# Optimization experiments

Measured on AMD Instinct MI355X. Metric: run time of the kernel, lower is better.

## Reference

```python
import jax, jax.numpy as jnp
import numpy as np

NUM_HEADS = 32
NUM_KV_HEADS = 8
HEAD_DIM = 128
SEQ = 2048
MAX_SLOTS = 4096
SCALE = float(1.0 / np.sqrt(HEAD_DIM))  # attn_scale
G = NUM_HEADS // NUM_KV_HEADS  # num_queries_per_kv


def setup_inputs() -> dict:
    key = jax.random.key(0)
    k1, k2, k3 = jax.random.split(key, 3)
    q = jax.random.normal(k1, (SEQ, NUM_HEADS, HEAD_DIM), dtype=jnp.float32)
    k = jax.random.normal(k2, (SEQ, NUM_KV_HEADS, HEAD_DIM), dtype=jnp.float32)
    v = jax.random.normal(k3, (SEQ, NUM_KV_HEADS, HEAD_DIM), dtype=jnp.float32)
    k_cache = jnp.zeros((MAX_SLOTS, NUM_KV_HEADS, HEAD_DIM), dtype=jnp.float32)
    v_cache = jnp.zeros((MAX_SLOTS, NUM_KV_HEADS, HEAD_DIM), dtype=jnp.float32)
    slot_mapping = jnp.arange(SEQ, dtype=jnp.int64)  # contiguous block_table slots
    return {"q": q, "k": k, "v": v, "k_cache": k_cache, "v_cache": v_cache,
            "slot_mapping": slot_mapping}


def reference(q, k, v, k_cache, v_cache, slot_mapping):
    # prefill: scatter-write new K/V into the paged cache (self.k_cache[slot_mapping] = k)
    kc = k_cache.at[slot_mapping].set(k)
    vc = v_cache.at[slot_mapping].set(v)
    # gather K/V back from the cache via slot mapping (paged gather pattern)
    k_attn = kc[slot_mapping]  # (S, Hkv, D) == k since slots are unique
    v_attn = vc[slot_mapping]
    # GQA: repeat_interleave kv heads to match query heads
    kr = jnp.repeat(k_attn, G, axis=1)  # (S, H, D)
    vr = jnp.repeat(v_attn, G, axis=1)
    # scores: (H, Sq, Sk), naive full materialization as in the original
    scores = jnp.einsum('qhd,khd->hqk', q, kr) * SCALE
    sq, sk = q.shape[0], k_attn.shape[0]
    mask = jnp.tril(jnp.ones((sq, sk), dtype=bool))  # causal (num_query_tokens > 1)
    scores = jnp.where(mask[None, :, :], scores, -jnp.inf)
    weights = jax.nn.softmax(scores, axis=-1)
    out = jnp.einsum('hqk,khd->qhd', weights, vr)  # (S, H, D)
    return out
```

## Files before the change

### kernel.cpp

```cpp
#include <hip/hip_runtime.h>
#include <hip/hip_bf16.h>

#define QSTRIDE 4096
#define KSTRIDE 1024
#define CSCALE 0.1275174364688796f

typedef __attribute__((ext_vector_type(8))) short short8;
typedef __attribute__((ext_vector_type(4))) float f32x4;

union S8U { short8 s; unsigned u[4]; };

__device__ __forceinline__ unsigned short f2bf(float f) {
    union { __hip_bfloat16 b; unsigned short u; } cv;
    cv.b = __float2bfloat16(f);
    return cv.u;
}

__launch_bounds__(256, 3)
__global__ void attn_fwd(const float* __restrict__ Qg,
                         const float* __restrict__ Kg,
                         const float* __restrict__ Vg,
                         float* __restrict__ Og) {
    const int bid = blockIdx.x;
    const int qb  = 31 - (bid >> 5);
    const int h   = bid & 31;
    const int hk  = h >> 2;
    const int tid  = threadIdx.x;
    const int w    = tid >> 6;
    const int lane = tid & 63;
    const int c16  = lane & 15;
    const int g    = lane >> 4;
    const int dg   = g * 8;

    __shared__ unsigned short Ks[64][136];
    __shared__ unsigned short Vt[128][72];

    const int q0w  = qb * 64 + w * 16;
    const int qrow = q0w + c16;

    short8 qf[4];
    {
        const float* qp = Qg + (size_t)qrow * QSTRIDE + h * 128 + dg;
        #pragma unroll
        for (int ks = 0; ks < 4; ++ks) {
            f32x4 a = *(const f32x4*)(qp + ks * 32);
            f32x4 b = *(const f32x4*)(qp + ks * 32 + 4);
            short8 f;
            f[0] = (short)f2bf(a[0] * CSCALE); f[1] = (short)f2bf(a[1] * CSCALE);
            f[2] = (short)f2bf(a[2] * CSCALE); f[3] = (short)f2bf(a[3] * CSCALE);
            f[4] = (short)f2bf(b[0] * CSCALE); f[5] = (short)f2bf(b[1] * CSCALE);
            f[6] = (short)f2bf(b[2] * CSCALE); f[7] = (short)f2bf(b[3] * CSCALE);
            qf[ks] = f;
        }
    }

    const int ka  = tid >> 5;
    const int kc  = (tid & 31) * 4;
    const int va  = tid & 15;
    const int vch = tid >> 4;

    f32x4 kreg[8], vreg[8];

    auto LOAD_T = [&](int t) {
        const float* kb = Kg + (size_t)(t * 64) * KSTRIDE + hk * 128;
        const float* vb = Vg + (size_t)(t * 64) * KSTRIDE + hk * 128;
        #pragma unroll
        for (int it = 0; it < 8; ++it)
            kreg[it] = *(const f32x4*)(kb + (ka + 8 * it) * KSTRIDE + kc);
        #pragma unroll
        for (int task = 0; task < 2; ++task) {
            #pragma unroll
            for (int j = 0; j < 4; ++j)
                vreg[task * 4 + j] =
                    *(const f32x4*)(vb + (4 * va + j) * KSTRIDE + (vch + 16 * task) * 4);
        }
    };

    auto WRITE_T = [&]() {
        #pragma unroll
        for (int it = 0; it < 8; ++it) {
            ushort4 u = make_ushort4(f2bf(kreg[it][0]), f2bf(kreg[it][1]),
                                     f2bf(kreg[it][2]), f2bf(kreg[it][3]));
            *(ushort4*)&Ks[ka + 8 * it][kc] = u;
        }
        #pragma unroll
        for (int task = 0; task < 2; ++task) {
            const int d0 = 4 * (vch + 16 * task);
            #pragma unroll
            for (int di = 0; di < 4; ++di) {
                ushort4 u = make_ushort4(f2bf(vreg[task * 4 + 0][di]),
                                         f2bf(vreg[task * 4 + 1][di]),
                                         f2bf(vreg[task * 4 + 2][di]),
                                         f2bf(vreg[task * 4 + 3][di]));
                *(ushort4*)&Vt[d0 + di][4 * va] = u;
            }
        }
    };

    f32x4 oacc[8];
    #pragma unroll
    for (int dt = 0; dt < 8; ++dt) oacc[dt] = (f32x4){0.f, 0.f, 0.f, 0.f};
    float m = -1e30f, l = 0.f;

    const int nt = qb + 1;
    LOAD_T(0);
    WRITE_T();
    if (nt > 1) LOAD_T(1);
    __syncthreads();

    for (int t = 0; t < nt; ++t) {
        const int kv0 = t * 64;

        f32x4 sacc[4];
        __builtin_amdgcn_s_setprio(1);
        #pragma unroll
        for (int ct = 0; ct < 4; ++ct) {
            f32x4 acc = (f32x4){0.f, 0.f, 0.f, 0.f};
            #pragma unroll
            for (int ks = 0; ks < 4; ++ks) {
                short8 kf = *(const short8*)&Ks[ct * 16 + c16][ks * 32 + dg];
                acc = __builtin_amdgcn_mfma_f32_16x16x32_bf16(kf, qf[ks], acc, 0, 0, 0);
            }
            sacc[ct] = acc;
        }
        __builtin_amdgcn_s_setprio(0);

        const bool needmask = (kv0 + 63) > q0w;
        float mx = -1e30f;
        #pragma unroll
        for (int ct = 0; ct < 4; ++ct) {
            #pragma unroll
            for (int r = 0; r < 4; ++r) {
                float s = sacc[ct][r];
                const int kv = kv0 + ct * 16 + 4 * g + r;
                if (needmask && kv > qrow) s = -1e30f;
                sacc[ct][r] = s;
                mx = fmaxf(mx, s);
            }
        }
        mx = fmaxf(mx, __shfl_xor(mx, 16));
        mx = fmaxf(mx, __shfl_xor(mx, 32));

        const float mn  = fmaxf(m, mx);
        const float fac = exp2f(m - mn);
        m = mn;

        float ps = 0.f;
        #pragma unroll
        for (int ct = 0; ct < 4; ++ct) {
            #pragma unroll
            for (int r = 0; r < 4; ++r) {
                float p = exp2f(sacc[ct][r] - m);
                sacc[ct][r] = p;
                ps += p;
            }
        }
        ps += __shfl_xor(ps, 16);
        ps += __shfl_xor(ps, 32);
        l = l * fac + ps;

        #pragma unroll
        for (int dt = 0; dt < 8; ++dt) {
            #pragma unroll
            for (int r = 0; r < 4; ++r) oacc[dt][r] *= fac;
        }

        unsigned pk[4][2];
        #pragma unroll
        for (int ct = 0; ct < 4; ++ct) {
            #pragma unroll
            for (int j = 0; j < 2; ++j)
                pk[ct][j] = (unsigned)f2bf(sacc[ct][2 * j]) |
                            ((unsigned)f2bf(sacc[ct][2 * j + 1]) << 16);
        }
        S8U pf0, pf1;
        {
            const int sb = ((g & 1) << 5) | c16;
            #pragma unroll
            for (int b = 0; b < 2; ++b) {
                const int src = sb + (b << 4);
                #pragma unroll
                for (int j = 0; j < 2; ++j) {
                    unsigned lo0 = (unsigned)__shfl((int)pk[0][j], src);
                    unsigned hi0 = (unsigned)__shfl((int)pk[1][j], src);
                    unsigned lo1 = (unsigned)__shfl((int)pk[2][j], src);
                    unsigned hi1 = (unsigned)__shfl((int)pk[3][j], src);
                    pf0.u[2 * b + j] = (g & 2) ? hi0 : lo0;
                    pf1.u[2 * b + j] = (g & 2) ? hi1 : lo1;
                }
            }
        }

        __builtin_amdgcn_s_setprio(1);
        #pragma unroll
        for (int dt = 0; dt < 8; ++dt) {
            short8 vfa = *(const short8*)&Vt[dt * 16 + c16][0 * 32 + dg];
            short8 vfb = *(const short8*)&Vt[dt * 16 + c16][1 * 32 + dg];
            oacc[dt] = __builtin_amdgcn_mfma_f32_16x16x32_bf16(vfa, pf0.s, oacc[dt], 0, 0, 0);
            oacc[dt] = __builtin_amdgcn_mfma_f32_16x16x32_bf16(vfb, pf1.s, oacc[dt], 0, 0, 0);
        }
        __builtin_amdgcn_s_setprio(0);

        if (t + 1 < nt) {
            __syncthreads();
            WRITE_T();
            if (t + 2 < nt) LOAD_T(t + 2);
            __syncthreads();
        }
    }

    const float rl = 1.0f / l;
    float* op = Og + (size_t)qrow * QSTRIDE + h * 128 + 4 * g;
    #pragma unroll
    for (int dt = 0; dt < 8; ++dt) {
        float4 o;
        o.x = oacc[dt][0] * rl; o.y = oacc[dt][1] * rl;
        o.z = oacc[dt][2] * rl; o.w = oacc[dt][3] * rl;
        *(float4*)(op + dt * 16) = o;
    }
}

extern "C" void kernel_launch(void* const* d_in, const int* in_sizes, int n_in,
                              void* d_out, int out_size, void* d_ws, size_t ws_size,
                              hipStream_t stream) {
    const float* q = (const float*)d_in[0];
    const float* k = (const float*)d_in[1];
    const float* v = (const float*)d_in[2];
    float* out = (float*)d_out;
    attn_fwd<<<dim3(1024), 256, 0, stream>>>(q, k, v, out);
}
```

Measured before the change: 104.1 us.

## Pre-convert K/V to bf16, use 32x32 MFMA with 128-row query tiles and async LDS loads

Two prep kernels convert K to bf16 in head-major layout and V to a transposed bf16 layout in the workspace. The attention kernel then uses 128-query blocks with 32x32x16 MFMAs and streams K/V tiles into swizzled double-buffered LDS via global_load_lds. It also adds a lazy rescale that skips the softmax correction when the running max barely changes, and an LDS-staged coalesced output store. The aim is to remove the repeated fp32 K/V loads and per-block conversion, and to raise MFMA efficiency. In exchange it adds two extra launches and workspace traffic, and occupancy drops to 2 blocks per CU.

```diff
diff --git a/kernel.cpp b/kernel.cpp
--- a/kernel.cpp
+++ b/kernel.cpp
@@ -1,14 +1,16 @@
 #include <hip/hip_runtime.h>
 #include <hip/hip_bf16.h>
 
-#define QSTRIDE 4096
-#define KSTRIDE 1024
+#define SEQ 2048
+#define QSTR 4096
+#define KSTR 1024
 #define CSCALE 0.1275174364688796f
 
-typedef __attribute__((ext_vector_type(8))) short short8;
-typedef __attribute__((ext_vector_type(4))) float f32x4;
-
-union S8U { short8 s; unsigned u[4]; };
+typedef __attribute__((ext_vector_type(8)))  short short8;
+typedef __attribute__((ext_vector_type(4)))  float f32x4;
+typedef __attribute__((ext_vector_type(16))) float f32x16;
+
+union PF8 { unsigned u[4]; short8 s; };
 
 __device__ __forceinline__ unsigned short f2bf(float f) {
     union { __hip_bfloat16 b; unsigned short u; } cv;
@@ -16,207 +18,267 @@
     return cv.u;
 }
 
-__launch_bounds__(256, 3)
+__device__ __forceinline__ void gload16(const unsigned short* g, unsigned short* l) {
+    __builtin_amdgcn_global_load_lds(
+        (const __attribute__((address_space(1))) void*)g,
+        (__attribute__((address_space(3))) void*)l, 16, 0, 0);
+}
+
+__global__ void prep_k(const float* __restrict__ Kg, unsigned short* __restrict__ Kb) {
+    int gi = blockIdx.x * 256 + threadIdx.x;
+    int kv = gi >> 8;
+    int rem = gi & 255;
+    int hk = rem >> 5;
+    int d4 = rem & 31;
+    f32x4 k4 = *(const f32x4*)(Kg + ((size_t)kv * 8 + hk) * 128 + 4 * d4);
+    ushort4 u = make_ushort4(f2bf(k4[0]), f2bf(k4[1]), f2bf(k4[2]), f2bf(k4[3]));
+    *(ushort4*)(Kb + ((size_t)hk * SEQ + kv) * 128 + 4 * d4) = u;
+}
+
+__global__ void prep_v(const float* __restrict__ Vg, unsigned short* __restrict__ Vtb) {
+    const int hk  = blockIdx.x >> 5;
+    const int kvb = blockIdx.x & 31;
+    __shared__ unsigned short T[128][72];
+    const int t = threadIdx.x;
+    #pragma unroll
+    for (int i = 0; i < 8; ++i) {
+        int idx = t + 256 * i;
+        int r = idx >> 5, d4 = idx & 31;
+        f32x4 v = *(const f32x4*)(Vg + ((size_t)(kvb * 64 + r) * 8 + hk) * 128 + 4 * d4);
+        T[4 * d4 + 0][r] = f2bf(v[0]);
+        T[4 * d4 + 1][r] = f2bf(v[1]);
+        T[4 * d4 + 2][r] = f2bf(v[2]);
+        T[4 * d4 + 3][r] = f2bf(v[3]);
+    }
+    __syncthreads();
+    #pragma unroll
+    for (int i = 0; i < 8; ++i) {
+        int idx = t + 256 * i;
+        int d = idx >> 4, c4 = idx & 15;
+        ushort4 u = *(ushort4*)&T[d][4 * c4];
+        *(ushort4*)(Vtb + ((size_t)hk * 128 + d) * SEQ + kvb * 64 + 4 * c4) = u;
+    }
+}
+
+__launch_bounds__(256, 2)
 __global__ void attn_fwd(const float* __restrict__ Qg,
-                         const float* __restrict__ Kg,
-                         const float* __restrict__ Vg,
+                         const unsigned short* __restrict__ Kb,
+                         const unsigned short* __restrict__ Vtb,
                          float* __restrict__ Og) {
-    const int bid = blockIdx.x;
-    const int qb  = 31 - (bid >> 5);
-    const int h   = bid & 31;
-    const int hk  = h >> 2;
+    const int bid  = blockIdx.x;
+    const int gidx = bid >> 5;
+    const int qb   = (gidx < 8) ? (15 - gidx) : (gidx - 8);
+    const int h    = bid & 31;
+    const int hk   = h >> 2;
     const int tid  = threadIdx.x;
     const int w    = tid >> 6;
     const int lane = tid & 63;
-    const int c16  = lane & 15;
-    const int g    = lane >> 4;
-    const int dg   = g * 8;
-
-    __shared__ unsigned short Ks[64][136];
-    __shared__ unsigned short Vt[128][72];
-
-    const int q0w  = qb * 64 + w * 16;
-    const int qrow = q0w + c16;
-
-    short8 qf[4];
+    const int q5   = lane & 31;
+    const int t5   = lane >> 5;
+    const int swz  = lane & 7;
+
+    __shared__ __align__(16) unsigned char smem[67584];
+    typedef unsigned short KsT[64][128];
+    typedef unsigned short VtT[128][64];
+    KsT* Ks = (KsT*)smem;
+    VtT* Vt = (VtT*)(smem + 32768);
+    float (*Ot)[132] = (float(*)[132])smem;
+
+    const int q0w = qb * 128 + 32 * w;
+    const int nt  = 2 * qb + 2;
+
+    short8 qf[8];
     {
-        const float* qp = Qg + (size_t)qrow * QSTRIDE + h * 128 + dg;
-        #pragma unroll
-        for (int ks = 0; ks < 4; ++ks) {
-            f32x4 a = *(const f32x4*)(qp + ks * 32);
-            f32x4 b = *(const f32x4*)(qp + ks * 32 + 4);
+        const float* qp = Qg + (size_t)(q0w + q5) * QSTR + h * 128 + 8 * t5;
+        #pragma unroll
+        for (int st = 0; st < 8; ++st) {
+            f32x4 a = *(const f32x4*)(qp + 16 * st);
+            f32x4 b = *(const f32x4*)(qp + 16 * st + 4);
             short8 f;
             f[0] = (short)f2bf(a[0] * CSCALE); f[1] = (short)f2bf(a[1] * CSCALE);
             f[2] = (short)f2bf(a[2] * CSCALE); f[3] = (short)f2bf(a[3] * CSCALE);
             f[4] = (short)f2bf(b[0] * CSCALE); f[5] = (short)f2bf(b[1] * CSCALE);
             f[6] = (short)f2bf(b[2] * CSCALE); f[7] = (short)f2bf(b[3] * CSCALE);
-            qf[ks] = f;
-        }
-    }
-
-    const int ka  = tid >> 5;
-    const int kc  = (tid & 31) * 4;
-    const int va  = tid & 15;
-    const int vch = tid >> 4;
-
-    f32x4 kreg[8], vreg[8];
-
-    auto LOAD_T = [&](int t) {
-        const float* kb = Kg + (size_t)(t * 64) * KSTRIDE + hk * 128;
-        const float* vb = Vg + (size_t)(t * 64) * KSTRIDE + hk * 128;
-        #pragma unroll
-        for (int it = 0; it < 8; ++it)
-            kreg[it] = *(const f32x4*)(kb + (ka + 8 * it) * KSTRIDE + kc);
-        #pragma unroll
-        for (int task = 0; task < 2; ++task) {
-            #pragma unroll
-            for (int j = 0; j < 4; ++j)
-                vreg[task * 4 + j] =
-                    *(const f32x4*)(vb + (4 * va + j) * KSTRIDE + (vch + 16 * task) * 4);
+            qf[st] = f;
+        }
+    }
+    #pragma unroll
+    for (int st = 0; st < 8; ++st) asm volatile("" :: "v"(qf[st]));
+    asm volatile("s_waitcnt vmcnt(0)" ::: "memory");
+
+    f32x16 oacc[4];
+    #pragma unroll
+    for (int dt = 0; dt < 4; ++dt)
+        #pragma unroll
+        for (int r = 0; r < 16; ++r) oacc[dt][r] = 0.f;
+    float m = -1e30f, l = 0.f;
+
+    auto ISSUE = [&](int t, int b) {
+        const int kv0 = t * 64;
+        #pragma unroll
+        for (int p = 0; p < 4; ++p) {
+            int row = 16 * w + 4 * p + (lane >> 4);
+            const unsigned short* g = Kb +
+                ((size_t)hk * SEQ + kv0 + row) * 128 + 8 * ((lane & 15) ^ (row & 7));
+            gload16(g, &Ks[b][16 * w + 4 * p][0]);
+        }
+        #pragma unroll
+        for (int p = 0; p < 4; ++p) {
+            int d = 32 * w + 8 * p + (lane >> 3);
+            const unsigned short* g = Vtb +
+                ((size_t)hk * 128 + d) * SEQ + kv0 + 8 * ((lane & 7) ^ (d & 7));
+            gload16(g, &Vt[b][32 * w + 8 * p][0]);
         }
     };
 
-    auto WRITE_T = [&]() {
-        #pragma unroll
-        for (int it = 0; it < 8; ++it) {
-            ushort4 u = make_ushort4(f2bf(kreg[it][0]), f2bf(kreg[it][1]),
-                                     f2bf(kreg[it][2]), f2bf(kreg[it][3]));
-            *(ushort4*)&Ks[ka + 8 * it][kc] = u;
-        }
-        #pragma unroll
-        for (int task = 0; task < 2; ++task) {
-            const int d0 = 4 * (vch + 16 * task);
-            #pragma unroll
-            for (int di = 0; di < 4; ++di) {
-                ushort4 u = make_ushort4(f2bf(vreg[task * 4 + 0][di]),
-                                         f2bf(vreg[task * 4 + 1][di]),
-                                         f2bf(vreg[task * 4 + 2][di]),
-                                         f2bf(vreg[task * 4 + 3][di]));
-                *(ushort4*)&Vt[d0 + di][4 * va] = u;
-            }
-        }
-    };
-
-    f32x4 oacc[8];
-    #pragma unroll
-    for (int dt = 0; dt < 8; ++dt) oacc[dt] = (f32x4){0.f, 0.f, 0.f, 0.f};
-    float m = -1e30f, l = 0.f;
-
-    const int nt = qb + 1;
-    LOAD_T(0);
-    WRITE_T();
-    if (nt > 1) LOAD_T(1);
-    __syncthreads();
+    ISSUE(0, 0);
+    if (nt > 1) ISSUE(1, 1);
 
     for (int t = 0; t < nt; ++t) {
         const int kv0 = t * 64;
-
-        f32x4 sacc[4];
-        __builtin_amdgcn_s_setprio(1);
-        #pragma unroll
-        for (int ct = 0; ct < 4; ++ct) {
-            f32x4 acc = (f32x4){0.f, 0.f, 0.f, 0.f};
+        const int buf = t & 1;
+        if (t + 1 < nt) asm volatile("s_waitcnt vmcnt(8)" ::: "memory");
+        else            asm volatile("s_waitcnt vmcnt(0)" ::: "memory");
+        __builtin_amdgcn_s_barrier();
+
+        const bool active = (kv0 <= q0w + 31);
+        if (active) {
+            f32x16 sac[2];
+            __builtin_amdgcn_s_setprio(1);
+            #pragma unroll
+            for (int kvs = 0; kvs < 2; ++kvs) {
+                f32x16 acc;
+                #pragma unroll
+                for (int r = 0; r < 16; ++r) acc[r] = 0.f;
+                #pragma unroll
+                for (int st = 0; st < 8; ++st) {
+                    short8 kf = *(const short8*)
+                        &Ks[buf][32 * kvs + q5][8 * ((2 * st + t5) ^ swz)];
+                    acc = __builtin_amdgcn_mfma_f32_32x32x16_bf16(kf, qf[st], acc, 0, 0, 0);
+                }
+                sac[kvs] = acc;
+            }
+            __builtin_amdgcn_s_setprio(0);
+
+            if (kv0 + 63 > q0w) {
+                const int qrow = q0w + q5;
+                #pragma unroll
+                for (int kvs = 0; kvs < 2; ++kvs)
+                    #pragma unroll
+                    for (int r = 0; r < 16; ++r) {
+                        int kv = kv0 + 32 * kvs + (r & 3) + 8 * (r >> 2) + 4 * t5;
+                        if (kv > qrow) sac[kvs][r] = -1e30f;
+                    }
+            }
+
+            float mx = sac[0][0];
+            #pragma unroll
+            for (int kvs = 0; kvs < 2; ++kvs)
+                #pragma unroll
+                for (int r = 0; r < 16; ++r) mx = fmaxf(mx, sac[kvs][r]);
+            mx = fmaxf(mx, __shfl_xor(mx, 32));
+
+            const bool skip = __all(mx <= m + 11.0f);
+            float fac = 1.0f;
+            if (!skip) {
+                float mn = fmaxf(m, mx);
+                fac = exp2f(m - mn);
+                m = mn;
+            }
+
+            float ps = 0.f;
+            #pragma unroll
+            for (int kvs = 0; kvs < 2; ++kvs)
+                #pragma unroll
+                for (int r = 0; r < 16; ++r) {
+                    float p = exp2f(sac[kvs][r] - m);
+                    sac[kvs][r] = p;
+                    ps += p;
+                }
+            ps += __shfl_xor(ps, 32);
+            if (!skip) {
+                l = l * fac + ps;
+                #pragma unroll
+                for (int dt = 0; dt < 4; ++dt)
+                    #pragma unroll
+                    for (int r = 0; r < 16; ++r) oacc[dt][r] *= fac;
+            } else {
+                l += ps;
+            }
+
+            unsigned pkw[2][8];
+            #pragma unroll
+            for (int a = 0; a < 2; ++a)
+                #pragma unroll
+                for (int rp = 0; rp < 8; ++rp)
+                    pkw[a][rp] = (unsigned)f2bf(sac[a][2 * rp]) |
+                                 ((unsigned)f2bf(sac[a][2 * rp + 1]) << 16);
+
+            unsigned xp[2][8];
+            #pragma unroll
+            for (int a = 0; a < 2; ++a)
+                #pragma unroll
+                for (int i = 0; i < 8; ++i)
+                    xp[a][i] = (unsigned)__shfl_xor((int)pkw[a][i], 32);
+
+            PF8 pf[4];
             #pragma unroll
             for (int ks = 0; ks < 4; ++ks) {
-                short8 kf = *(const short8*)&Ks[ct * 16 + c16][ks * 32 + dg];
-                acc = __builtin_amdgcn_mfma_f32_16x16x32_bf16(kf, qf[ks], acc, 0, 0, 0);
-            }
-            sacc[ct] = acc;
-        }
-        __builtin_amdgcn_s_setprio(0);
-
-        const bool needmask = (kv0 + 63) > q0w;
-        float mx = -1e30f;
-        #pragma unroll
-        for (int ct = 0; ct < 4; ++ct) {
-            #pragma unroll
-            for (int r = 0; r < 4; ++r) {
-                float s = sacc[ct][r];
-                const int kv = kv0 + ct * 16 + 4 * g + r;
-                if (needmask && kv > qrow) s = -1e30f;
-                sacc[ct][r] = s;
-                mx = fmaxf(mx, s);
-            }
-        }
-        mx = fmaxf(mx, __shfl_xor(mx, 16));
-        mx = fmaxf(mx, __shfl_xor(mx, 32));
-
-        const float mn  = fmaxf(m, mx);
-        const float fac = exp2f(m - mn);
-        m = mn;
-
-        float ps = 0.f;
-        #pragma unroll
-        for (int ct = 0; ct < 4; ++ct) {
-            #pragma unroll
-            for (int r = 0; r < 4; ++r) {
-                float p = exp2f(sacc[ct][r] - m);
-                sacc[ct][r] = p;
-                ps += p;
-            }
-        }
-        ps += __shfl_xor(ps, 16);
-        ps += __shfl_xor(ps, 32);
-        l = l * fac + ps;
-
-        #pragma unroll
-        for (int dt = 0; dt < 8; ++dt) {
-            #pragma unroll
-            for (int r = 0; r < 4; ++r) oacc[dt][r] *= fac;
-        }
-
-        unsigned pk[4][2];
-        #pragma unroll
-        for (int ct = 0; ct < 4; ++ct) {
-            #pragma unroll
-            for (int j = 0; j < 2; ++j)
-                pk[ct][j] = (unsigned)f2bf(sacc[ct][2 * j]) |
-                            ((unsigned)f2bf(sacc[ct][2 * j + 1]) << 16);
-        }
-        S8U pf0, pf1;
-        {
-            const int sb = ((g & 1) << 5) | c16;
-            #pragma unroll
-            for (int b = 0; b < 2; ++b) {
-                const int src = sb + (b << 4);
-                #pragma unroll
-                for (int j = 0; j < 2; ++j) {
-                    unsigned lo0 = (unsigned)__shfl((int)pk[0][j], src);
-                    unsigned hi0 = (unsigned)__shfl((int)pk[1][j], src);
-                    unsigned lo1 = (unsigned)__shfl((int)pk[2][j], src);
-                    unsigned hi1 = (unsigned)__shfl((int)pk[3][j], src);
-                    pf0.u[2 * b + j] = (g & 2) ? hi0 : lo0;
-                    pf1.u[2 * b + j] = (g & 2) ? hi1 : lo1;
-                }
-            }
-        }
-
-        __builtin_amdgcn_s_setprio(1);
-        #pragma unroll
-        for (int dt = 0; dt < 8; ++dt) {
-            short8 vfa = *(const short8*)&Vt[dt * 16 + c16][0 * 32 + dg];
-            short8 vfb = *(const short8*)&Vt[dt * 16 + c16][1 * 32 + dg];
-            oacc[dt] = __builtin_amdgcn_mfma_f32_16x16x32_bf16(vfa, pf0.s, oacc[dt], 0, 0, 0);
-            oacc[dt] = __builtin_amdgcn_mfma_f32_16x16x32_bf16(vfb, pf1.s, oacc[dt], 0, 0, 0);
-        }
-        __builtin_amdgcn_s_setprio(0);
-
-        if (t + 1 < nt) {
-            __syncthreads();
-            WRITE_T();
-            if (t + 2 < nt) LOAD_T(t + 2);
-            __syncthreads();
-        }
-    }
-
+                const int a = ks >> 1;
+                #pragma unroll
+                for (int j = 0; j < 4; ++j) {
+                    const int ib = (j & 1) + 4 * (ks & 1);
+                    const unsigned own_lo = pkw[a][ib];
+                    const unsigned own_hi = pkw[a][ib + 2];
+                    const unsigned par_lo = xp[a][ib];
+                    const unsigned par_hi = xp[a][ib + 2];
+                    pf[ks].u[j] = (j < 2) ? (t5 ? par_hi : own_lo)
+                                          : (t5 ? own_hi : par_lo);
+                }
+            }
+
+            __builtin_amdgcn_s_setprio(1);
+            #pragma unroll
+            for (int dt = 0; dt < 4; ++dt) {
+                #pragma unroll
+                for (int ks = 0; ks < 4; ++ks) {
+                    short8 vf = *(const short8*)
+                        &Vt[buf][32 * dt + q5][8 * ((2 * ks + t5) ^ swz)];
+                    oacc[dt] = __builtin_amdgcn_mfma_f32_32x32x16_bf16(vf, pf[ks].s, oacc[dt], 0, 0, 0);
+                }
+            }
+            __builtin_amdgcn_s_setprio(0);
+        }
+
+        asm volatile("" ::: "memory");
+        __builtin_amdgcn_s_barrier();
+        if (t + 2 < nt) ISSUE(t + 2, buf);
+    }
+
+    asm volatile("" ::: "memory");
     const float rl = 1.0f / l;
-    float* op = Og + (size_t)qrow * QSTRIDE + h * 128 + 4 * g;
-    #pragma unroll
-    for (int dt = 0; dt < 8; ++dt) {
-        float4 o;
-        o.x = oacc[dt][0] * rl; o.y = oacc[dt][1] * rl;
-        o.z = oacc[dt][2] * rl; o.w = oacc[dt][3] * rl;
-        *(float4*)(op + dt * 16) = o;
+    #pragma unroll
+    for (int dt = 0; dt < 4; ++dt)
+        #pragma unroll
+        for (int b = 0; b < 4; ++b) {
+            f32x4 v;
+            v[0] = oacc[dt][4 * b + 0] * rl;
+            v[1] = oacc[dt][4 * b + 1] * rl;
+            v[2] = oacc[dt][4 * b + 2] * rl;
+            v[3] = oacc[dt][4 * b + 3] * rl;
+            *(f32x4*)&Ot[32 * w + q5][32 * dt + 8 * b + 4 * t5] = v;
+        }
+    __syncthreads();
+    {
+        const int col4 = (tid & 31) * 4;
+        const int r0   = tid >> 5;
+        float* ob = Og + (size_t)(qb * 128) * QSTR + h * 128;
+        #pragma unroll
+        for (int i = 0; i < 16; ++i) {
+            int row = 8 * i + r0;
+            f32x4 v = *(const f32x4*)&Ot[row][col4];
+            *(f32x4*)(ob + (size_t)row * QSTR + col4) = v;
+        }
     }
 }
 
@@ -227,5 +289,9 @@
     const float* k = (const float*)d_in[1];
     const float* v = (const float*)d_in[2];
     float* out = (float*)d_out;
-    attn_fwd<<<dim3(1024), 256, 0, stream>>>(q, k, v, out);
-}
+    unsigned short* Kb  = (unsigned short*)d_ws;
+    unsigned short* Vtb = Kb + (size_t)8 * SEQ * 128;
+    prep_k<<<dim3(2048), 256, 0, stream>>>(k, Kb);
+    prep_v<<<dim3(256), 256, 0, stream>>>(v, Vtb);
+    attn_fwd<<<dim3(512), 256, 0, stream>>>(q, Kb, Vtb, out);
+}
```

After: 89.37 us. -14.1%, faster.
